# Kernel tuning notes

Measured on AMD Instinct MI355X. Metric: run time of the kernel, lower is better.

## Reference

```python
import jax, jax.numpy as jnp
import numpy as np

B, T, C, HS = 8, 2048, 1024, 64
NEG_INF = float('-inf')


def setup_inputs() -> dict:
    key = jax.random.key(0)
    kx, kk, kq, kv = jax.random.split(key, 4)
    scale = 1.0 / np.sqrt(C)
    return {
        'x': jax.random.normal(kx, (B, T, C), dtype=jnp.float32),
        'Wk': jax.random.normal(kk, (C, HS), dtype=jnp.float32) * scale,
        'Wq': jax.random.normal(kq, (C, HS), dtype=jnp.float32) * scale,
        'Wv': jax.random.normal(kv, (C, HS), dtype=jnp.float32) * scale,
    }


def reference(x, Wk, Wq, Wv):
    b, t, c = x.shape
    k = x @ Wk          # [b, t, hs]
    q = x @ Wq          # [b, t, hs]
    v = x @ Wv          # [b, t, hs]
    # NOTE: original scales by c**-0.5 where c = input embed dim (not head_size)
    wei = jnp.einsum('bth,bsh->bts', q, k) * (c ** -0.5)  # [b, t(query), t(key)]
    # causal mask: position (i, j) valid iff j <= i
    causal = jnp.tril(jnp.ones((t, t), dtype=bool))
    wei = jnp.where(causal, wei, NEG_INF)
    # NOTE: original applies softmax over dim=1 (the QUERY axis) — reproduced faithfully
    wei = jax.nn.softmax(wei, axis=1)
    # dropout p=0.0 / eval mode -> identity
    return jnp.einsum('bts,bsh->bth', wei, v)  # [b, t, hs]
```

## Files before the change

### kernel.cpp

```cpp
#include <hip/hip_runtime.h>
#include <hip/hip_bf16.h>

namespace {

typedef unsigned short u16;
typedef __attribute__((ext_vector_type(8))) short bf16x8;
typedef __attribute__((ext_vector_type(4))) float f32x4;

constexpr int kB = 8, kT = 2048, kC = 1024, kH = 64;
constexpr float kScale = 0.03125f;

constexpr size_t kWtOff = 0;
constexpr size_t kQbOff = kWtOff + 3 * 64 * 1024;
constexpr size_t kKbOff = kQbOff + (size_t)16384 * 64;
constexpr size_t kVtOff = kKbOff + (size_t)16384 * 64;
constexpr size_t kLOff  = kVtOff + (size_t)16384 * 64;
constexpr size_t kPartOff = kLOff + (size_t)16384 * 2;

__device__ __forceinline__ u16 f2bu(float f) {
  __hip_bfloat16 h = __float2bfloat16(f);
  return *reinterpret_cast<u16*>(&h);
}
__device__ __forceinline__ float bu2f(unsigned int u) {
  union { unsigned int i; float f; } w;
  w.i = u << 16;
  return w.f;
}
__device__ __forceinline__ f32x4 mfma16(bf16x8 a, bf16x8 b, f32x4 c) {
  return __builtin_amdgcn_mfma_f32_16x16x32_bf16(a, b, c, 0, 0, 0);
}

__global__ __launch_bounds__(256) void zero_l_kernel(float* __restrict__ l) {
  l[blockIdx.x * 256 + threadIdx.x] = 0.f;
}

__global__ __launch_bounds__(256) void wt_kernel(
    const float* __restrict__ Wk, const float* __restrict__ Wq,
    const float* __restrict__ Wv, u16* __restrict__ Wt) {
  __shared__ float wsm[64 * 65];
  const int c0 = blockIdx.x * 64;
  const int mat = blockIdx.y;
  const float* W = (mat == 0) ? Wk : (mat == 1) ? Wq : Wv;
  const int tid = threadIdx.x;
#pragma unroll
  for (int ii = 0; ii < 4; ++ii) {
    const int p = tid + 256 * ii;
    const int row = p >> 4, col4 = p & 15;
    const float4 wv = *reinterpret_cast<const float4*>(&W[(size_t)(c0 + row) * 64 + col4 * 4]);
    wsm[row * 65 + col4 * 4 + 0] = wv.x;
    wsm[row * 65 + col4 * 4 + 1] = wv.y;
    wsm[row * 65 + col4 * 4 + 2] = wv.z;
    wsm[row * 65 + col4 * 4 + 3] = wv.w;
  }
  __syncthreads();
  const int h = tid & 63, seg = tid >> 6;
#pragma unroll
  for (int i = 0; i < 16; ++i) {
    const int c = seg * 16 + i;
    Wt[((size_t)mat * 64 + h) * 1024 + c0 + c] = f2bu(wsm[c * 65 + h]);
  }
}

__global__ __launch_bounds__(256) void qkv_kernel(
    const float* __restrict__ x, const u16* __restrict__ Wt,
    u16* __restrict__ qb, u16* __restrict__ kb, u16* __restrict__ vt) {
  __shared__ u16 wl[192 * 128];
  __shared__ u16 xl[32 * 128];
  const int tid = threadIdx.x;
  const int lane = tid & 63, w = tid >> 6;
  const int l15 = lane & 15, l4 = lane >> 4;
  const int m0 = blockIdx.x * 32;

  f32x4 acc[2][3];
#pragma unroll
  for (int mi = 0; mi < 2; ++mi)
#pragma unroll
    for (int ni = 0; ni < 3; ++ni) acc[mi][ni] = f32x4{0.f, 0.f, 0.f, 0.f};

  for (int p = 0; p < 8; ++p) {
    const int k0 = p * 128;
    __syncthreads();
#pragma unroll
    for (int i = 0; i < 12; ++i) {
      const int q = tid + 256 * i;
      const int row = q >> 4, c8 = (q & 15) * 8;
      const uint4 wv = *reinterpret_cast<const uint4*>(&Wt[(size_t)row * 1024 + k0 + c8]);
      *reinterpret_cast<uint4*>(&wl[(row * 128 + c8) ^ ((row & 7) << 3)]) = wv;
    }
#pragma unroll
    for (int i = 0; i < 4; ++i) {
      const int q = tid + 256 * i;
      const int row = q >> 5, c4 = (q & 31) * 4;
      const float4 xv = *reinterpret_cast<const float4*>(&x[(size_t)(m0 + row) * kC + k0 + c4]);
      uint2 pk;
      pk.x = (unsigned)f2bu(xv.x) | ((unsigned)f2bu(xv.y) << 16);
      pk.y = (unsigned)f2bu(xv.z) | ((unsigned)f2bu(xv.w) << 16);
      *reinterpret_cast<uint2*>(&xl[(row * 128 + c4) ^ ((row & 7) << 3)]) = pk;
    }
    __syncthreads();
#pragma unroll
    for (int ks = 0; ks < 4; ++ks) {
      const int kk = ks * 32 + 8 * l4;
      bf16x8 a[2];
#pragma unroll
      for (int mi = 0; mi < 2; ++mi) {
        const int row = 16 * mi + l15;
        a[mi] = *reinterpret_cast<const bf16x8*>(&xl[(row * 128 + kk) ^ ((row & 7) << 3)]);
      }
#pragma unroll
      for (int ni = 0; ni < 3; ++ni) {
        const int row = 48 * w + 16 * ni + l15;
        const bf16x8 bfr =
            *reinterpret_cast<const bf16x8*>(&wl[(row * 128 + kk) ^ ((row & 7) << 3)]);
#pragma unroll
        for (int mi = 0; mi < 2; ++mi) acc[mi][ni] = mfma16(a[mi], bfr, acc[mi][ni]);
      }
    }
  }
#pragma unroll
  for (int ni = 0; ni < 3; ++ni) {
    const int ncol = 48 * w + 16 * ni + l15;
    const int mat = ncol >> 6, h = ncol & 63;
#pragma unroll
    for (int mi = 0; mi < 2; ++mi) {
#pragma unroll
      for (int r = 0; r < 4; ++r) {
        const int m = m0 + 16 * mi + 4 * l4 + r;
        const u16 val = f2bu(acc[mi][ni][r]);
        if (mat == 0) kb[(size_t)m * 64 + h] = val;
        else if (mat == 1) qb[(size_t)m * 64 + h] = val;
        else vt[((size_t)((m >> 11) * 64 + h)) * 2048 + (m & 2047)] = val;
      }
    }
  }
}

__global__ __launch_bounds__(256) void colsum_kernel(
    const u16* __restrict__ qb, const u16* __restrict__ kb, float* __restrict__ lG) {
  const int bid = blockIdx.x;
  const int b = bid & 7;
  const int rr = bid >> 3;
  const int s0 = (rr & 31) * 64;
  const int tc = (rr >> 5) * 512;
  if (tc + 511 < s0) return;
  const int tid = threadIdx.x;
  const int lane = tid & 63, w = tid >> 6;
  const int l15 = lane & 15, l4 = lane >> 4;

  bf16x8 ka[4][2];
#pragma unroll
  for (int i = 0; i < 4; ++i) {
    const u16* kp = kb + (size_t)(b * kT + s0 + 16 * i + l15) * 64 + 8 * l4;
    ka[i][0] = *reinterpret_cast<const bf16x8*>(kp);
    ka[i][1] = *reinterpret_cast<const bf16x8*>(kp + 32);
  }
  f32x4 cs[4];
#pragma unroll
  for (int i = 0; i < 4; ++i) cs[i] = f32x4{0.f, 0.f, 0.f, 0.f};

  const int d0 = s0 - tc - 128 * w;
  const int jstart = (d0 > 0) ? (d0 >> 4) : 0;
  const u16* qbase = qb + (size_t)(b * kT + tc + 128 * w + l15) * 64 + 8 * l4;
  bf16x8 qf0, qf1;
  if (jstart < 8) {
    qf0 = *reinterpret_cast<const bf16x8*>(qbase + (size_t)jstart * 1024);
    qf1 = *reinterpret_cast<const bf16x8*>(qbase + (size_t)jstart * 1024 + 32);
  }
  for (int j = jstart; j < 8; ++j) {
    bf16x8 qn0, qn1;
    if (j < 7) {
      qn0 = *reinterpret_cast<const bf16x8*>(qbase + (size_t)(j + 1) * 1024);
      qn1 = *reinterpret_cast<const bf16x8*>(qbase + (size_t)(j + 1) * 1024 + 32);
    }
    const int t = tc + 128 * w + 16 * j + l15;
#pragma unroll
    for (int i = 0; i < 4; ++i) {
      f32x4 d = f32x4{0.f, 0.f, 0.f, 0.f};
      d = mfma16(ka[i][0], qf0, d);
      d = mfma16(ka[i][1], qf1, d);
#pragma unroll
      for (int r = 0; r < 4; ++r) {
        const int s = s0 + 16 * i + 4 * l4 + r;
        if (t >= s) cs[i][r] += __expf(d[r] * kScale);
      }
    }
    qf0 = qn0; qf1 = qn1;
  }
#pragma unroll
  for (int i = 0; i < 4; ++i) {
#pragma unroll
    for (int r = 0; r < 4; ++r) {
      float v = cs[i][r];
      v += __shfl_xor(v, 1, 64);
      v += __shfl_xor(v, 2, 64);
      v += __shfl_xor(v, 4, 64);
      v += __shfl_xor(v, 8, 64);
      if (l15 == 0) atomicAdd(&lG[b * kT + s0 + 16 * i + 4 * l4 + r], v);
    }
  }
}

__global__ __launch_bounds__(256) void vscale_kernel(
    u16* __restrict__ vt, const float* __restrict__ lG) {
  const int idx = blockIdx.x * 256 + threadIdx.x;
  const int row = idx >> 8;
  const int tc = (idx & 255) * 8;
  const int b = row >> 6;
  u16* vp = vt + (size_t)row * 2048 + tc;
  uint4 pv = *reinterpret_cast<const uint4*>(vp);
  const float* lp = lG + b * 2048 + tc;
  const float4 la = *reinterpret_cast<const float4*>(lp);
  const float4 lb = *reinterpret_cast<const float4*>(lp + 4);
  uint4 ov;
  ov.x = (unsigned)f2bu(bu2f(pv.x & 0xffffu) / la.x) |
         ((unsigned)f2bu(bu2f(pv.x >> 16) / la.y) << 16);
  ov.y = (unsigned)f2bu(bu2f(pv.y & 0xffffu) / la.z) |
         ((unsigned)f2bu(bu2f(pv.y >> 16) / la.w) << 16);
  ov.z = (unsigned)f2bu(bu2f(pv.z & 0xffffu) / lb.x) |
         ((unsigned)f2bu(bu2f(pv.z >> 16) / lb.y) << 16);
  ov.w = (unsigned)f2bu(bu2f(pv.w & 0xffffu) / lb.z) |
         ((unsigned)f2bu(bu2f(pv.w >> 16) / lb.w) << 16);
  *reinterpret_cast<uint4*>(vp) = ov;
}

__global__ __launch_bounds__(512, 4) void out_part_kernel(
    const u16* __restrict__ qb, const u16* __restrict__ kb, const u16* __restrict__ vt,
    float* __restrict__ part) {
  __shared__ u16 kl[64 * 64];
  __shared__ u16 vl[64 * 64];
  const int bid = blockIdx.x;
  const int b = bid & 7;
  const int q4 = (bid >> 3) & 3;
  const int tt = bid >> 5;
  const int t0 = tt * 128;
  const int tid = threadIdx.x;
  const int lane = tid & 63, w = tid >> 6;
  const int l15 = lane & 15, l4 = lane >> 4;
  const size_t bT = (size_t)b * kT;
  const int sA = l15 + 32 * (l4 & 1);
  const int sB = sA + 16;
  const bool hi = l4 >= 2;
  const int srow = tid >> 3, sc8 = (tid & 7) * 8;
  const int sidx = (srow * 64 + sc8) ^ ((srow & 7) << 3);

  const int tw = t0 + 16 * w;
  const u16* qp = qb + (bT + tw + l15) * 64 + 8 * l4;
  const bf16x8 qf0 = *reinterpret_cast<const bf16x8*>(qp);
  const bf16x8 qf1 = *reinterpret_cast<const bf16x8*>(qp + 32);

  f32x4 acc[4];
#pragma unroll
  for (int nf = 0; nf < 4; ++nf) acc[nf] = f32x4{0.f, 0.f, 0.f, 0.f};

  const int js0 = q4 * 8;
  const int js1 = min(js0 + 8, 2 * tt + 2);
  for (int js = js0; js < js1; ++js) {
    const int s0 = js * 64;
    __syncthreads();
    *reinterpret_cast<uint4*>(&kl[sidx]) =
        *reinterpret_cast<const uint4*>(&kb[(bT + s0 + srow) * 64 + sc8]);
    *reinterpret_cast<uint4*>(&vl[sidx]) =
        *reinterpret_cast<const uint4*>(&vt[(size_t)(b * 64 + srow) * kT + s0 + sc8]);
    __syncthreads();
    if (tw + 15 < s0) continue;

    unsigned pk0[4], pk1[4];
    const int t = tw + l15;
    const bool masked = (s0 + 63 > tw);
#pragma unroll
    for (int jf = 0; jf < 4; ++jf) {
      const int krow = 16 * jf + l15;
      const bf16x8 kf0 = *reinterpret_cast<const bf16x8*>(
          &kl[(krow * 64 + 8 * l4) ^ ((krow & 7) << 3)]);
      const bf16x8 kf1 = *reinterpret_cast<const bf16x8*>(
          &kl[(krow * 64 + 32 + 8 * l4) ^ ((krow & 7) << 3)]);
      f32x4 d = f32x4{0.f, 0.f, 0.f, 0.f};
      d = mfma16(kf0, qf0, d);
      d = mfma16(kf1, qf1, d);
      float p[4];
      if (masked) {
        const int sb = s0 + 16 * jf + 4 * l4;
#pragma unroll
        for (int r = 0; r < 4; ++r) p[r] = (t >= sb + r) ? __expf(d[r] * kScale) : 0.f;
      } else {
#pragma unroll
        for (int r = 0; r < 4; ++r) p[r] = __expf(d[r] * kScale);
      }
      pk0[jf] = (unsigned)f2bu(p[0]) | ((unsigned)f2bu(p[1]) << 16);
      pk1[jf] = (unsigned)f2bu(p[2]) | ((unsigned)f2bu(p[3]) << 16);
    }
    {
      const unsigned a0 = __shfl(pk0[0], sA), a1 = __shfl(pk1[0], sA);
      const unsigned a2 = __shfl(pk0[0], sB), a3 = __shfl(pk1[0], sB);
      const unsigned b0 = __shfl(pk0[1], sA), b1 = __shfl(pk1[1], sA);
      const unsigned b2 = __shfl(pk0[1], sB), b3 = __shfl(pk1[1], sB);
      uint4 pw;
      pw.x = hi ? b0 : a0; pw.y = hi ? b1 : a1;
      pw.z = hi ? b2 : a2; pw.w = hi ? b3 : a3;
      const bf16x8 pa = *reinterpret_cast<const bf16x8*>(&pw);
#pragma unroll
      for (int nf = 0; nf < 4; ++nf) {
        const int vrow = 16 * nf + l15;
        const bf16x8 vf = *reinterpret_cast<const bf16x8*>(
            &vl[(vrow * 64 + 8 * l4) ^ ((vrow & 7) << 3)]);
        acc[nf] = mfma16(pa, vf, acc[nf]);
      }
    }
    {
      const unsigned a0 = __shfl(pk0[2], sA), a1 = __shfl(pk1[2], sA);
      const unsigned a2 = __shfl(pk0[2], sB), a3 = __shfl(pk1[2], sB);
      const unsigned b0 = __shfl(pk0[3], sA), b1 = __shfl(pk1[3], sA);
      const unsigned b2 = __shfl(pk0[3], sB), b3 = __shfl(pk1[3], sB);
      uint4 pw;
      pw.x = hi ? b0 : a0; pw.y = hi ? b1 : a1;
      pw.z = hi ? b2 : a2; pw.w = hi ? b3 : a3;
      const bf16x8 pa = *reinterpret_cast<const bf16x8*>(&pw);
#pragma unroll
      for (int nf = 0; nf < 4; ++nf) {
        const int vrow = 16 * nf + l15;
        const bf16x8 vf = *reinterpret_cast<const bf16x8*>(
            &vl[(vrow * 64 + 32 + 8 * l4) ^ ((vrow & 7) << 3)]);
        acc[nf] = mfma16(pa, vf, acc[nf]);
      }
    }
  }
  float* pb = part + (size_t)(q4 * 8 + b) * kT * kH;
#pragma unroll
  for (int nf = 0; nf < 4; ++nf) {
#pragma unroll
    for (int r = 0; r < 4; ++r) {
      pb[(size_t)(tw + 4 * l4 + r) * 64 + 16 * nf + l15] = acc[nf][r];
    }
  }
}

__global__ __launch_bounds__(256) void combine_kernel(
    const float* __restrict__ part, float* __restrict__ out) {
  const size_t i = ((size_t)blockIdx.x * 256 + threadIdx.x) * 4;
  const float4 p0 = *reinterpret_cast<const float4*>(part + i);
  const float4 p1 = *reinterpret_cast<const float4*>(part + 1048576 + i);
  const float4 p2 = *reinterpret_cast<const float4*>(part + 2097152 + i);
  const float4 p3 = *reinterpret_cast<const float4*>(part + 3145728 + i);
  float4 s;
  s.x = p0.x + p1.x + p2.x + p3.x;
  s.y = p0.y + p1.y + p2.y + p3.y;
  s.z = p0.z + p1.z + p2.z + p3.z;
  s.w = p0.w + p1.w + p2.w + p3.w;
  *reinterpret_cast<float4*>(out + i) = s;
}

}

extern "C" void kernel_launch(void* const* d_in, const int* in_sizes, int n_in,
                              void* d_out, int out_size, void* d_ws, size_t ws_size,
                              hipStream_t stream) {
  const float* x = (const float*)d_in[0];
  const float* Wk = (const float*)d_in[1];
  const float* Wq = (const float*)d_in[2];
  const float* Wv = (const float*)d_in[3];
  u16* wsu = (u16*)d_ws;
  u16* Wt = wsu + kWtOff;
  u16* qb = wsu + kQbOff;
  u16* kb = wsu + kKbOff;
  u16* vt = wsu + kVtOff;
  float* lG = (float*)(wsu + kLOff);
  float* part = (float*)(wsu + kPartOff);
  float* out = (float*)d_out;

  zero_l_kernel<<<dim3(kB * kT / 256), dim3(256), 0, stream>>>(lG);
  wt_kernel<<<dim3(16, 3), dim3(256), 0, stream>>>(Wk, Wq, Wv, Wt);
  qkv_kernel<<<dim3(kB * kT / 32), dim3(256), 0, stream>>>(x, Wt, qb, kb, vt);
  colsum_kernel<<<dim3(1024), dim3(256), 0, stream>>>(qb, kb, lG);
  vscale_kernel<<<dim3(512), dim3(256), 0, stream>>>(vt, lG);
  out_part_kernel<<<dim3(512), dim3(512), 0, stream>>>(qb, kb, vt, part);
  combine_kernel<<<dim3(1024), dim3(256), 0, stream>>>(part, out);
}
```

Baseline: 76.41 us.

## Fuse V column-normalization into attention kernel and prefetch QKV GEMM tiles

Removes the separate vscale kernel, which read, divided and rewrote all of V by the softmax column sums. The out_part kernel now loads those sums and multiplies each exp value by its reciprocal, computed with the fast rcp instruction. The QKV projection kernel also gains register double-buffering, loading the next K-slice of weights and x into registers while the MFMAs run on the current shared-memory tile. This saves one launch and a full pass over V, at the cost of more registers in qkv_kernel and extra loads and rcp work inside the attention loop.

```diff
diff --git a/kernel.cpp b/kernel.cpp
--- a/kernel.cpp
+++ b/kernel.cpp
@@ -20,11 +20,6 @@
 __device__ __forceinline__ u16 f2bu(float f) {
   __hip_bfloat16 h = __float2bfloat16(f);
   return *reinterpret_cast<u16*>(&h);
-}
-__device__ __forceinline__ float bu2f(unsigned int u) {
-  union { unsigned int i; float f; } w;
-  w.i = u << 16;
-  return w.f;
 }
 __device__ __forceinline__ f32x4 mfma16(bf16x8 a, bf16x8 b, f32x4 c) {
   return __builtin_amdgcn_mfma_f32_16x16x32_bf16(a, b, c, 0, 0, 0);
@@ -77,27 +72,53 @@
 #pragma unroll
     for (int ni = 0; ni < 3; ++ni) acc[mi][ni] = f32x4{0.f, 0.f, 0.f, 0.f};
 
+  uint4 wreg[12];
+  float4 xreg[4];
+#pragma unroll
+  for (int i = 0; i < 12; ++i) {
+    const int q = tid + 256 * i;
+    const int row = q >> 4, c8 = (q & 15) * 8;
+    wreg[i] = *reinterpret_cast<const uint4*>(&Wt[(size_t)row * 1024 + c8]);
+  }
+#pragma unroll
+  for (int i = 0; i < 4; ++i) {
+    const int q = tid + 256 * i;
+    const int row = q >> 5, c4 = (q & 31) * 4;
+    xreg[i] = *reinterpret_cast<const float4*>(&x[(size_t)(m0 + row) * kC + c4]);
+  }
+#pragma unroll
+  for (int i = 0; i < 12; ++i) {
+    const int q = tid + 256 * i;
+    const int row = q >> 4, c8 = (q & 15) * 8;
+    *reinterpret_cast<uint4*>(&wl[(row * 128 + c8) ^ ((row & 7) << 3)]) = wreg[i];
+  }
+#pragma unroll
+  for (int i = 0; i < 4; ++i) {
+    const int q = tid + 256 * i;
+    const int row = q >> 5, c4 = (q & 31) * 4;
+    uint2 pk;
+    pk.x = (unsigned)f2bu(xreg[i].x) | ((unsigned)f2bu(xreg[i].y) << 16);
+    pk.y = (unsigned)f2bu(xreg[i].z) | ((unsigned)f2bu(xreg[i].w) << 16);
+    *reinterpret_cast<uint2*>(&xl[(row * 128 + c4) ^ ((row & 7) << 3)]) = pk;
+  }
+  __syncthreads();
+
   for (int p = 0; p < 8; ++p) {
-    const int k0 = p * 128;
-    __syncthreads();
-#pragma unroll
-    for (int i = 0; i < 12; ++i) {
-      const int q = tid + 256 * i;
-      const int row = q >> 4, c8 = (q & 15) * 8;
-      const uint4 wv = *reinterpret_cast<const uint4*>(&Wt[(size_t)row * 1024 + k0 + c8]);
-      *reinterpret_cast<uint4*>(&wl[(row * 128 + c8) ^ ((row & 7) << 3)]) = wv;
-    }
-#pragma unroll
-    for (int i = 0; i < 4; ++i) {
-      const int q = tid + 256 * i;
-      const int row = q >> 5, c4 = (q & 31) * 4;
-      const float4 xv = *reinterpret_cast<const float4*>(&x[(size_t)(m0 + row) * kC + k0 + c4]);
-      uint2 pk;
-      pk.x = (unsigned)f2bu(xv.x) | ((unsigned)f2bu(xv.y) << 16);
-      pk.y = (unsigned)f2bu(xv.z) | ((unsigned)f2bu(xv.w) << 16);
-      *reinterpret_cast<uint2*>(&xl[(row * 128 + c4) ^ ((row & 7) << 3)]) = pk;
-    }
-    __syncthreads();
+    if (p < 7) {
+      const int k1 = (p + 1) * 128;
+#pragma unroll
+      for (int i = 0; i < 12; ++i) {
+        const int q = tid + 256 * i;
+        const int row = q >> 4, c8 = (q & 15) * 8;
+        wreg[i] = *reinterpret_cast<const uint4*>(&Wt[(size_t)row * 1024 + k1 + c8]);
+      }
+#pragma unroll
+      for (int i = 0; i < 4; ++i) {
+        const int q = tid + 256 * i;
+        const int row = q >> 5, c4 = (q & 31) * 4;
+        xreg[i] = *reinterpret_cast<const float4*>(&x[(size_t)(m0 + row) * kC + k1 + c4]);
+      }
+    }
 #pragma unroll
     for (int ks = 0; ks < 4; ++ks) {
       const int kk = ks * 32 + 8 * l4;
@@ -115,6 +136,25 @@
 #pragma unroll
         for (int mi = 0; mi < 2; ++mi) acc[mi][ni] = mfma16(a[mi], bfr, acc[mi][ni]);
       }
+    }
+    if (p < 7) {
+      __syncthreads();
+#pragma unroll
+      for (int i = 0; i < 12; ++i) {
+        const int q = tid + 256 * i;
+        const int row = q >> 4, c8 = (q & 15) * 8;
+        *reinterpret_cast<uint4*>(&wl[(row * 128 + c8) ^ ((row & 7) << 3)]) = wreg[i];
+      }
+#pragma unroll
+      for (int i = 0; i < 4; ++i) {
+        const int q = tid + 256 * i;
+        const int row = q >> 5, c4 = (q & 31) * 4;
+        uint2 pk;
+        pk.x = (unsigned)f2bu(xreg[i].x) | ((unsigned)f2bu(xreg[i].y) << 16);
+        pk.y = (unsigned)f2bu(xreg[i].z) | ((unsigned)f2bu(xreg[i].w) << 16);
+        *reinterpret_cast<uint2*>(&xl[(row * 128 + c4) ^ ((row & 7) << 3)]) = pk;
+      }
+      __syncthreads();
     }
   }
 #pragma unroll
@@ -200,32 +240,9 @@
   }
 }
 
-__global__ __launch_bounds__(256) void vscale_kernel(
-    u16* __restrict__ vt, const float* __restrict__ lG) {
-  const int idx = blockIdx.x * 256 + threadIdx.x;
-  const int row = idx >> 8;
-  const int tc = (idx & 255) * 8;
-  const int b = row >> 6;
-  u16* vp = vt + (size_t)row * 2048 + tc;
-  uint4 pv = *reinterpret_cast<const uint4*>(vp);
-  const float* lp = lG + b * 2048 + tc;
-  const float4 la = *reinterpret_cast<const float4*>(lp);
-  const float4 lb = *reinterpret_cast<const float4*>(lp + 4);
-  uint4 ov;
-  ov.x = (unsigned)f2bu(bu2f(pv.x & 0xffffu) / la.x) |
-         ((unsigned)f2bu(bu2f(pv.x >> 16) / la.y) << 16);
-  ov.y = (unsigned)f2bu(bu2f(pv.y & 0xffffu) / la.z) |
-         ((unsigned)f2bu(bu2f(pv.y >> 16) / la.w) << 16);
-  ov.z = (unsigned)f2bu(bu2f(pv.z & 0xffffu) / lb.x) |
-         ((unsigned)f2bu(bu2f(pv.z >> 16) / lb.y) << 16);
-  ov.w = (unsigned)f2bu(bu2f(pv.w & 0xffffu) / lb.z) |
-         ((unsigned)f2bu(bu2f(pv.w >> 16) / lb.w) << 16);
-  *reinterpret_cast<uint4*>(vp) = ov;
-}
-
 __global__ __launch_bounds__(512, 4) void out_part_kernel(
     const u16* __restrict__ qb, const u16* __restrict__ kb, const u16* __restrict__ vt,
-    float* __restrict__ part) {
+    const float* __restrict__ lG, float* __restrict__ part) {
   __shared__ u16 kl[64 * 64];
   __shared__ u16 vl[64 * 64];
   const int bid = blockIdx.x;
@@ -264,6 +281,11 @@
     __syncthreads();
     if (tw + 15 < s0) continue;
 
+    float4 lv[4];
+#pragma unroll
+    for (int jf = 0; jf < 4; ++jf)
+      lv[jf] = *reinterpret_cast<const float4*>(&lG[bT + s0 + 16 * jf + 4 * l4]);
+
     unsigned pk0[4], pk1[4];
     const int t = tw + l15;
     const bool masked = (s0 + 63 > tw);
@@ -277,14 +299,22 @@
       f32x4 d = f32x4{0.f, 0.f, 0.f, 0.f};
       d = mfma16(kf0, qf0, d);
       d = mfma16(kf1, qf1, d);
+      const float rl0 = __builtin_amdgcn_rcpf(lv[jf].x);
+      const float rl1 = __builtin_amdgcn_rcpf(lv[jf].y);
+      const float rl2 = __builtin_amdgcn_rcpf(lv[jf].z);
+      const float rl3 = __builtin_amdgcn_rcpf(lv[jf].w);
       float p[4];
       if (masked) {
         const int sb = s0 + 16 * jf + 4 * l4;
-#pragma unroll
-        for (int r = 0; r < 4; ++r) p[r] = (t >= sb + r) ? __expf(d[r] * kScale) : 0.f;
+        p[0] = (t >= sb + 0) ? __expf(d[0] * kScale) * rl0 : 0.f;
+        p[1] = (t >= sb + 1) ? __expf(d[1] * kScale) * rl1 : 0.f;
+        p[2] = (t >= sb + 2) ? __expf(d[2] * kScale) * rl2 : 0.f;
+        p[3] = (t >= sb + 3) ? __expf(d[3] * kScale) * rl3 : 0.f;
       } else {
-#pragma unroll
-        for (int r = 0; r < 4; ++r) p[r] = __expf(d[r] * kScale);
+        p[0] = __expf(d[0] * kScale) * rl0;
+        p[1] = __expf(d[1] * kScale) * rl1;
+        p[2] = __expf(d[2] * kScale) * rl2;
+        p[3] = __expf(d[3] * kScale) * rl3;
       }
       pk0[jf] = (unsigned)f2bu(p[0]) | ((unsigned)f2bu(p[1]) << 16);
       pk1[jf] = (unsigned)f2bu(p[2]) | ((unsigned)f2bu(p[3]) << 16);
@@ -371,7 +401,6 @@
   wt_kernel<<<dim3(16, 3), dim3(256), 0, stream>>>(Wk, Wq, Wv, Wt);
   qkv_kernel<<<dim3(kB * kT / 32), dim3(256), 0, stream>>>(x, Wt, qb, kb, vt);
   colsum_kernel<<<dim3(1024), dim3(256), 0, stream>>>(qb, kb, lG);
-  vscale_kernel<<<dim3(512), dim3(256), 0, stream>>>(vt, lG);
-  out_part_kernel<<<dim3(512), dim3(512), 0, stream>>>(qb, kb, vt, part);
+  out_part_kernel<<<dim3(512), dim3(512), 0, stream>>>(qb, kb, vt, lG, part);
   combine_kernel<<<dim3(1024), dim3(256), 0, stream>>>(part, out);
 }
```

Measured after the change: 118.0 us. 1.54x slower.
